# Optimization experiments

Measured on AMD Instinct MI355X. Metric: run time of the kernel, lower is better.

## Reference

```python
import jax, jax.numpy as jnp
import numpy as np

NUM_HEADS = 8
KEY_DIM = 512  # d_gain = 1/sqrt(key_dim) in the original (NOT per-head dim)
MASK_FILL = -1000000.0


def setup_inputs() -> dict:
    key = jax.random.key(0)
    ks = jax.random.split(key, 6)
    N, Tq, Tk, D, U = 8, 1024, 1024, 512, 512
    query = jax.random.normal(ks[0], (N, Tq, D), dtype=jnp.float32)
    key_t = jax.random.normal(ks[1], (N, Tk, D), dtype=jnp.float32)
    key_mask = jax.random.randint(ks[2], (N, Tk), 0, 2).astype(bool)
    Wq = jax.random.normal(ks[3], (D, U), dtype=jnp.float32) / np.sqrt(D)
    Wk = jax.random.normal(ks[4], (D, U), dtype=jnp.float32) / np.sqrt(D)
    Wv = jax.random.normal(ks[5], (D, U), dtype=jnp.float32) / np.sqrt(D)
    return {"query": query, "key": key_t, "key_mask": key_mask,
            "Wq": Wq, "Wk": Wk, "Wv": Wv}


def reference(query, key, key_mask, Wq, Wk, Wv):
    N, Tq, _ = query.shape
    Tk = key.shape[1]
    U = Wq.shape[1]
    h = NUM_HEADS
    d = U // h
    scale = 1.0 / (KEY_DIM ** 0.5)

    # projections then split heads: [N,T,U] -> [h,N,T,d]
    q = (query @ Wq).reshape(N, Tq, h, d).transpose(2, 0, 1, 3)
    k = (key @ Wk).reshape(N, Tk, h, d).transpose(2, 0, 1, 3)
    v = (key @ Wv).reshape(N, Tk, h, d).transpose(2, 0, 1, 3)

    scores = scale * jnp.einsum('hnqd,hnkd->hnqk', q, k)
    scores = jnp.where(key_mask[None, :, None, :], scores, MASK_FILL)
    attn = jax.nn.softmax(scores, axis=3)
    out = jnp.einsum('hnqk,hnkd->hnqd', attn, v)
    # merge heads: [h,N,Tq,d] -> [N,Tq,h*d]
    return out.transpose(1, 2, 0, 3).reshape(N, Tq, U)
```

## Files before the change

### kernel.cpp

```cpp
#include <hip/hip_runtime.h>
#include <hip/hip_bf16.h>

typedef unsigned short u16;
typedef __attribute__((ext_vector_type(8))) short short8;
typedef __attribute__((ext_vector_type(4))) short short4v;
typedef __attribute__((ext_vector_type(4))) float f32x4;

#define NB 8
#define TT 1024
#define DD 512
#define UU 512
#define HH 8
#define DH 64
#define SCALE 0.044194173824159216f
#define LOG2E 1.4426950408889634f
#define MASK_FILL_2 -1442695.0f

__device__ __forceinline__ float ld_flex(const void* p, long i, bool f32) {
  if (f32) return ((const float*)p)[i];
  unsigned int u = (unsigned int)(((const u16*)p)[i]) << 16;
  return __uint_as_float(u);
}

__device__ __forceinline__ u16 f32_to_bf16(float f) {
  unsigned int u = __float_as_uint(f);
  unsigned int r = (u + 0x7FFFu + ((u >> 16) & 1u)) >> 16;
  return (u16)r;
}

__device__ __forceinline__ float ex2(float x) {
#if __has_builtin(__builtin_amdgcn_exp2f)
  return __builtin_amdgcn_exp2f(x);
#else
  return __expf(x * 0.6931471805599453f);
#endif
}

__device__ __forceinline__ unsigned int pk_bf16(float a, float b) {
  union { __hip_bfloat162 h2; unsigned int u; } c;
  c.h2 = __float22bfloat162_rn(make_float2(a, b));
  return c.u;
}

__device__ __forceinline__ void gld16(const void* g, void* l) {
  __builtin_amdgcn_global_load_lds(
      (const __attribute__((address_space(1))) unsigned int*)g,
      (__attribute__((address_space(3))) unsigned int*)l, 16, 0, 0);
}

#define CONV_BLOCKS 8192
#define WT_BLOCKS 768
#define MASK_BLOCKS 32

__global__ __launch_bounds__(256) void prep_kernel(
    const void* __restrict__ query, const void* __restrict__ key,
    const void* __restrict__ W0, const void* __restrict__ W1,
    const void* __restrict__ W2, const void* __restrict__ mask,
    u16* __restrict__ Xq, u16* __restrict__ Xk, u16* __restrict__ Wt,
    float* __restrict__ maskadd, int* __restrict__ flags) {
  __shared__ float tile[32][33];
  __shared__ int s_f32, s_mi32;
  const int b = blockIdx.x, tid = threadIdx.x;

  if (tid == 0) { s_f32 = 0; s_mi32 = 1; }
  __syncthreads();
  {
    const u16* qh = (const u16*)query;
    int weird = 0;
#pragma unroll
    for (int p = 0; p < 4; ++p) {
      unsigned int u = (unsigned int)qh[tid * 4 + p] << 16;
      float v = __uint_as_float(u);
      if (!(v == v) || fabsf(v) > 1e6f) weird = 1;
    }
    if (weird) atomicOr(&s_f32, 1);
    const unsigned int* mi = (const unsigned int*)mask;
    if (mi[tid * 2] > 1u || mi[tid * 2 + 1] > 1u) atomicAnd(&s_mi32, 0);
  }
  __syncthreads();
  const bool f32 = s_f32 != 0;
  const bool mi32 = s_mi32 != 0;
  if (b == CONV_BLOCKS && tid == 0) { flags[0] = s_f32; flags[1] = s_mi32; }

  if (b < CONV_BLOCKS) {
    if (!f32) return;
    const void* in = (b < 4096) ? query : key;
    u16* out = (b < 4096) ? Xq : Xk;
    int i = (b & 4095) * 256 + tid;
    float4 v = ((const float4*)in)[i];
    ushort4 o;
    o.x = f32_to_bf16(v.x); o.y = f32_to_bf16(v.y);
    o.z = f32_to_bf16(v.z); o.w = f32_to_bf16(v.w);
    ((ushort4*)out)[i] = o;
  } else if (b < CONV_BLOCKS + WT_BLOCKS) {
    const int lb = b - CONV_BLOCKS;
    const int z = lb >> 8, rem = lb & 255;
    const int k0 = (rem & 15) * 32, n0 = (rem >> 4) * 32;
    const void* W = (z == 0) ? W0 : (z == 1) ? W1 : W2;
    const float sc = (z == 0) ? SCALE * LOG2E : 1.0f;
    u16* out = Wt + (size_t)z * DD * UU;
#pragma unroll
    for (int p = 0; p < 4; ++p) {
      int i = (tid >> 5) + p * 8, j = tid & 31;
      tile[i][j] = ld_flex(W, (long)(k0 + i) * UU + n0 + j, f32);
    }
    __syncthreads();
#pragma unroll
    for (int p = 0; p < 4; ++p) {
      int nl = (tid >> 5) + p * 8, kl = tid & 31;
      out[(size_t)(n0 + nl) * DD + k0 + kl] = f32_to_bf16(tile[kl][nl] * sc);
    }
  } else {
    const int i = (b - CONV_BLOCKS - WT_BLOCKS) * 256 + tid;
    bool mv = mi32 ? (((const int*)mask)[i] != 0)
                   : (((const unsigned char*)mask)[i] != 0);
    maskadd[i] = mv ? 0.0f : MASK_FILL_2;
  }
}

__global__ __launch_bounds__(256) void proj_mfma(
    const void* __restrict__ query, const void* __restrict__ key,
    const u16* __restrict__ Xq, const u16* __restrict__ Xk,
    const u16* __restrict__ Wt, u16* __restrict__ Qp, u16* __restrict__ Kp,
    u16* __restrict__ Vt, const int* __restrict__ flags) {
  __shared__ __align__(16) u16 smem[128 * 136];
  const bool f32 = flags[0] != 0;
  const int lid = blockIdx.x + (blockIdx.y << 6) + (blockIdx.z << 8);
  const int swz = (lid & 7) * 96 + (lid >> 3);
  const int bx = swz & 63, by = (swz >> 6) & 3, z = swz >> 8;
  const u16* X = (z == 0) ? (f32 ? Xq : (const u16*)query)
                          : (f32 ? Xk : (const u16*)key);
  const u16* Wz = Wt + (size_t)z * DD * UU;
  const int m0 = bx * 128, n0 = by * 128;
  const int tid = threadIdx.x;
  const int w = tid >> 6, l = tid & 63;
  const int quad = l >> 4, l15 = l & 15;
  const int wm = (w >> 1) * 64, wn = (w & 1) * 64;

  const int c0 = w * 128 + l;
  const int row0 = c0 >> 2, q0 = (c0 & 3) * 8;
  const int c1 = c0 + 64;
  const int row1 = c1 >> 2, q1 = (c1 & 3) * 8;
  const u16* aS0 = X + (size_t)(m0 + row0) * DD + q0;
  const u16* aS1 = X + (size_t)(m0 + row1) * DD + q1;
  const u16* bS0 = Wz + (size_t)(n0 + row0) * DD + q0;
  const u16* bS1 = Wz + (size_t)(n0 + row1) * DD + q1;
  const int dD0 = w * 1024;
  const int dD1 = w * 1024 + 512;

  f32x4 acc[4][4];
#pragma unroll
  for (int mi = 0; mi < 4; ++mi)
#pragma unroll
    for (int ni = 0; ni < 4; ++ni)
#pragma unroll
      for (int r = 0; r < 4; ++r) acc[mi][ni][r] = 0.0f;

  gld16(aS0, smem + dD0);
  gld16(aS1, smem + dD1);
  gld16(bS0, smem + 4096 + dD0);
  gld16(bS1, smem + 4096 + dD1);

#pragma unroll 1
  for (int t = 0; t < 16; ++t) {
    const int co = (t & 1) * 8192;
    if (t < 15) {
      const int k1 = (t + 1) * 32;
      const int no = ((t + 1) & 1) * 8192;
      gld16(aS0 + k1, smem + no + dD0);
      gld16(aS1 + k1, smem + no + dD1);
      gld16(bS0 + k1, smem + no + 4096 + dD0);
      gld16(bS1 + k1, smem + no + 4096 + dD1);
      asm volatile("s_waitcnt vmcnt(4)" ::: "memory");
    } else {
      asm volatile("s_waitcnt vmcnt(0)" ::: "memory");
    }
    __builtin_amdgcn_s_barrier();

    short8 af[4], bf[4];
#pragma unroll
    for (int mi = 0; mi < 4; ++mi)
      af[mi] = *(const short8*)&smem[co + (wm + mi * 16 + l15) * 32 + quad * 8];
#pragma unroll
    for (int ni = 0; ni < 4; ++ni)
      bf[ni] = *(const short8*)&smem[co + 4096 + (wn + ni * 16 + l15) * 32 + quad * 8];
#pragma unroll
    for (int mi = 0; mi < 4; ++mi)
#pragma unroll
      for (int ni = 0; ni < 4; ++ni)
        acc[mi][ni] = __builtin_amdgcn_mfma_f32_16x16x32_bf16(
            af[mi], bf[ni], acc[mi][ni], 0, 0, 0);
    __builtin_amdgcn_s_barrier();
  }

  if (z < 2) {
#pragma unroll
    for (int mi = 0; mi < 4; ++mi)
#pragma unroll
      for (int ni = 0; ni < 4; ++ni) {
        const int ml = wm + mi * 16 + quad * 4;
        const int nl = wn + ni * 16 + l15;
#pragma unroll
        for (int r = 0; r < 4; ++r)
          smem[(ml + r) * 136 + nl] = f32_to_bf16(acc[mi][ni][r]);
      }
  } else {
#pragma unroll
    for (int mi = 0; mi < 4; ++mi)
#pragma unroll
      for (int ni = 0; ni < 4; ++ni) {
        const int ml = wm + mi * 16 + quad * 4;
        const int nl = wn + ni * 16 + l15;
        ushort4 pk;
        pk.x = f32_to_bf16(acc[mi][ni][0]);
        pk.y = f32_to_bf16(acc[mi][ni][1]);
        pk.z = f32_to_bf16(acc[mi][ni][2]);
        pk.w = f32_to_bf16(acc[mi][ni][3]);
        *(ushort4*)&smem[nl * 136 + ml] = pk;
      }
  }
  __syncthreads();

  if (z < 2) {
    u16* outp = (z == 0) ? Qp : Kp;
#pragma unroll
    for (int p = 0; p < 8; ++p) {
      const int idx = tid + p * 256;
      const int row = idx >> 4, c8 = (idx & 15) * 8;
      short8 v = *(const short8*)&smem[row * 136 + c8];
      *(short8*)&outp[(size_t)(m0 + row) * UU + n0 + c8] = v;
    }
  } else {
    const int nb = m0 >> 10, tk0 = m0 & 1023;
#pragma unroll
    for (int p = 0; p < 8; ++p) {
      const int idx = tid + p * 256;
      const int row = idx >> 4, c8 = (idx & 15) * 8;
      const int u = n0 + row, h = u >> 6, dh = u & 63;
      short8 v = *(const short8*)&smem[row * 136 + c8];
      *(short8*)&Vt[(size_t)((nb * HH + h) * DH + dh) * TT + tk0 + c8] = v;
    }
  }
}

__global__ __launch_bounds__(256) void attn_mfma(
    const u16* __restrict__ Qp, const u16* __restrict__ Kp,
    const u16* __restrict__ Vt, const float* __restrict__ maskadd,
    void* __restrict__ out, const int* __restrict__ flags) {
  __shared__ __align__(16) char smem[23040];
  const int tid = threadIdx.x;
  const int w = tid >> 6, l = tid & 63;
  const int quad = l >> 4, l15 = l & 15;
  const int lid = blockIdx.x + (blockIdx.y << 4) + (blockIdx.z << 7);
  const int swz = (lid & 7) * 128 + (lid >> 3);
  const int qt = swz & 15, h = (swz >> 4) & 7, n = swz >> 7;
  const int qsub = w >> 1, ks = w & 1;
  const int q0 = qt * 64 + qsub * 32;
  const int kb0 = ks * 512;
  const bool f32o = flags[0] != 0;
  u16* Pw = (u16*)smem + w * 2304;
  float* lp = (float*)(smem + 18432);
  float* s_mask = (float*)(smem + 18944);

  ((float4*)s_mask)[tid] = ((const float4*)(maskadd + n * TT))[tid];

  const u16* qbase = Qp + (size_t)(n * TT + q0 + l15) * UU + h * DH + quad * 8;
  short8 bq[2][2];
  bq[0][0] = *(const short8*)(qbase);
  bq[0][1] = *(const short8*)(qbase + 32);
  bq[1][0] = *(const short8*)(qbase + 16 * UU);
  bq[1][1] = *(const short8*)(qbase + 16 * UU + 32);

  const u16* kbase = Kp + (size_t)(n * TT + l15) * UU + h * DH + quad * 8;
  const u16* vbase = Vt + (size_t)((n * HH + h) * DH + l15) * TT + quad * 8;

  f32x4 o[2][4];
  float lsum[2] = {0.0f, 0.0f};
#pragma unroll
  for (int nq = 0; nq < 2; ++nq)
#pragma unroll
    for (int ni = 0; ni < 4; ++ni)
#pragma unroll
      for (int r = 0; r < 4; ++r) o[nq][ni][r] = 0.0f;

  __syncthreads();

  short8 ak[2][2];
#pragma unroll
  for (int kt = 0; kt < 2; ++kt)
#pragma unroll
    for (int kd = 0; kd < 2; ++kd)
      ak[kt][kd] = *(const short8*)(kbase + (size_t)(kb0 + kt * 16) * UU + kd * 32);
  {
    f32x4 s[2][2];
#pragma unroll
    for (int kt = 0; kt < 2; ++kt)
#pragma unroll
      for (int nq = 0; nq < 2; ++nq) {
#pragma unroll
        for (int r = 0; r < 4; ++r) s[kt][nq][r] = 0.0f;
#pragma unroll
        for (int kd = 0; kd < 2; ++kd)
          s[kt][nq] = __builtin_amdgcn_mfma_f32_16x16x32_bf16(
              ak[kt][kd], bq[nq][kd], s[kt][nq], 0, 0, 0);
      }
#pragma unroll
    for (int kt = 0; kt < 2; ++kt)
#pragma unroll
      for (int kd = 0; kd < 2; ++kd)
        ak[kt][kd] = *(const short8*)(kbase + (size_t)(kb0 + 32 + kt * 16) * UU + kd * 32);
    float4 mk[2];
    mk[0] = *(const float4*)&s_mask[kb0 + quad * 4];
    mk[1] = *(const float4*)&s_mask[kb0 + 16 + quad * 4];
#pragma unroll
    for (int kt = 0; kt < 2; ++kt)
#pragma unroll
      for (int nq = 0; nq < 2; ++nq) {
        float e0 = ex2(s[kt][nq][0] + mk[kt].x);
        float e1 = ex2(s[kt][nq][1] + mk[kt].y);
        float e2 = ex2(s[kt][nq][2] + mk[kt].z);
        float e3 = ex2(s[kt][nq][3] + mk[kt].w);
        lsum[nq] += (e0 + e1) + (e2 + e3);
        uint2 pk = make_uint2(pk_bf16(e0, e1), pk_bf16(e2, e3));
        *(uint2*)&Pw[(nq * 16 + l15) * 36 + kt * 16 + quad * 4] = pk;
      }
  }

#pragma unroll 1
  for (int it = 0; it < 16; ++it) {
    const int kb = kb0 + it * 32;
    u16* Pr = Pw + (it & 1) * 1152;
    short8 ap[2];
#pragma unroll
    for (int nq = 0; nq < 2; ++nq) {
      short4v lo = *(const short4v*)&Pr[(nq * 16 + l15) * 36 + quad * 8];
      short4v hi = *(const short4v*)&Pr[(nq * 16 + l15) * 36 + quad * 8 + 4];
      union { short8 v8; short4v v4[2]; } u;
      u.v4[0] = lo; u.v4[1] = hi;
      ap[nq] = u.v8;
    }
    short8 vf[4];
#pragma unroll
    for (int ni = 0; ni < 4; ++ni)
      vf[ni] = *(const short8*)(vbase + (size_t)(ni * 16) * TT + kb);
    __builtin_amdgcn_sched_barrier(0);

    if (it < 15) {
      f32x4 s[2][2];
#pragma unroll
      for (int kt = 0; kt < 2; ++kt)
#pragma unroll
        for (int nq = 0; nq < 2; ++nq) {
#pragma unroll
          for (int r = 0; r < 4; ++r) s[kt][nq][r] = 0.0f;
#pragma unroll
          for (int kd = 0; kd < 2; ++kd)
            s[kt][nq] = __builtin_amdgcn_mfma_f32_16x16x32_bf16(
                ak[kt][kd], bq[nq][kd], s[kt][nq], 0, 0, 0);
        }
      if (it < 14) {
        const int kb2 = kb + 64;
#pragma unroll
        for (int kt = 0; kt < 2; ++kt)
#pragma unroll
          for (int kd = 0; kd < 2; ++kd)
            ak[kt][kd] = *(const short8*)(kbase + (size_t)(kb2 + kt * 16) * UU + kd * 32);
      }
      float4 mk[2];
      mk[0] = *(const float4*)&s_mask[kb + 32 + quad * 4];
      mk[1] = *(const float4*)&s_mask[kb + 48 + quad * 4];
      u16* Pn = Pw + ((it + 1) & 1) * 1152;
#pragma unroll
      for (int kt = 0; kt < 2; ++kt)
#pragma unroll
        for (int nq = 0; nq < 2; ++nq) {
          float e0 = ex2(s[kt][nq][0] + mk[kt].x);
          float e1 = ex2(s[kt][nq][1] + mk[kt].y);
          float e2 = ex2(s[kt][nq][2] + mk[kt].z);
          float e3 = ex2(s[kt][nq][3] + mk[kt].w);
          lsum[nq] += (e0 + e1) + (e2 + e3);
          uint2 pk = make_uint2(pk_bf16(e0, e1), pk_bf16(e2, e3));
          *(uint2*)&Pn[(nq * 16 + l15) * 36 + kt * 16 + quad * 4] = pk;
        }
    }
    __builtin_amdgcn_sched_barrier(0);

#pragma unroll
    for (int nq = 0; nq < 2; ++nq)
#pragma unroll
      for (int ni = 0; ni < 4; ++ni)
        o[nq][ni] = __builtin_amdgcn_mfma_f32_16x16x32_bf16(
            ap[nq], vf[ni], o[nq][ni], 0, 0, 0);
  }

#pragma unroll
  for (int nq = 0; nq < 2; ++nq) {
    lsum[nq] += __shfl_xor(lsum[nq], 16);
    lsum[nq] += __shfl_xor(lsum[nq], 32);
  }

  if (quad == 0) {
    lp[w * 32 + l15] = lsum[0];
    lp[w * 32 + 16 + l15] = lsum[1];
  }
  __syncthreads();

  float* cbuf = (float*)smem;
#pragma unroll
  for (int c = 0; c < 4; ++c) {
    if ((w >> 1) == (c >> 1)) {
      float* Ow = cbuf + (w & 1) * (16 * 68);
#pragma unroll
      for (int ni = 0; ni < 4; ++ni)
#pragma unroll
        for (int r = 0; r < 4; ++r)
          Ow[(quad * 4 + r) * 68 + ni * 16 + l15] = o[c & 1][ni][r];
    }
    __syncthreads();
    for (int i = tid; i < 16 * 64; i += 256) {
      int q = i >> 6, j = i & 63;
      float s = cbuf[q * 68 + j] + cbuf[1088 + q * 68 + j];
      int qg = c * 16 + q;
      int base = (c >> 1) * 64;
      float lsum2 = lp[base + (qg & 31)] + lp[base + 32 + (qg & 31)];
      float v = s / lsum2;
      size_t idx = (size_t)(n * TT + qt * 64 + qg) * UU + h * DH + j;
      if (f32o) ((float*)out)[idx] = v;
      else ((u16*)out)[idx] = f32_to_bf16(v);
    }
    __syncthreads();
  }
}

extern "C" void kernel_launch(void* const* d_in, const int* in_sizes, int n_in,
                              void* d_out, int out_size, void* d_ws, size_t ws_size,
                              hipStream_t stream) {
  const void* query = d_in[0];
  const void* key   = d_in[1];
  const void* mask  = d_in[2];
  const void* Wq    = d_in[3];
  const void* Wk    = d_in[4];
  const void* Wv    = d_in[5];

  char* base = (char*)d_ws;
  int* flags = (int*)base;
  float* maskadd = (float*)(base + 256);
  u16* Wt  = (u16*)(base + 64 * 1024);
  u16* Xq  = Wt + (size_t)3 * DD * UU;
  u16* Xk  = Xq + (size_t)NB * TT * DD;
  u16* Qp  = Xk + (size_t)NB * TT * DD;
  u16* Kp  = Qp + (size_t)NB * TT * UU;
  u16* Vtp = Kp + (size_t)NB * TT * UU;

  prep_kernel<<<CONV_BLOCKS + WT_BLOCKS + MASK_BLOCKS, 256, 0, stream>>>(
      query, key, Wq, Wk, Wv, mask, Xq, Xk, Wt, maskadd, flags);

  dim3 pgrid(NB * TT / 128, UU / 128, 3);
  proj_mfma<<<pgrid, 256, 0, stream>>>(query, key, Xq, Xk, Wt, Qp, Kp, Vtp, flags);

  dim3 agrid(TT / 64, HH, NB);
  attn_mfma<<<agrid, 256, 0, stream>>>(Qp, Kp, Vtp, maskadd, d_out, flags);
}
```

Before: 180.5 us.

## Stage K/V tiles in LDS with double-buffered async loads, drop split-K combine

The attention kernel is restructured so each of the 4 warps owns 16 query rows over the full key range, instead of 32 rows over half the keys. Each 32-key K tile and V tile is loaded once per block into XOR-swizzled, double-buffered LDS with direct global-to-LDS loads, rather than every warp fetching its own fragments from global memory. This removes redundant global traffic and the LDS-based cross-warp reduction epilogue, and outputs are written straight from registers. In exchange it adds two block barriers per 32-key step over 32 steps, and it requests 4 blocks per CU through launch bounds, which may constrain register allocation.

```diff
diff --git a/kernel.cpp b/kernel.cpp
--- a/kernel.cpp
+++ b/kernel.cpp
@@ -243,193 +243,138 @@
   }
 }
 
-__global__ __launch_bounds__(256) void attn_mfma(
+__global__ __launch_bounds__(256, 4) void attn_mfma(
     const u16* __restrict__ Qp, const u16* __restrict__ Kp,
     const u16* __restrict__ Vt, const float* __restrict__ maskadd,
     void* __restrict__ out, const int* __restrict__ flags) {
-  __shared__ __align__(16) char smem[23040];
+  __shared__ __align__(16) char smem[25344];
+  u16* sU = (u16*)smem;
   const int tid = threadIdx.x;
   const int w = tid >> 6, l = tid & 63;
   const int quad = l >> 4, l15 = l & 15;
   const int lid = blockIdx.x + (blockIdx.y << 4) + (blockIdx.z << 7);
   const int swz = (lid & 7) * 128 + (lid >> 3);
   const int qt = swz & 15, h = (swz >> 4) & 7, n = swz >> 7;
-  const int qsub = w >> 1, ks = w & 1;
-  const int q0 = qt * 64 + qsub * 32;
-  const int kb0 = ks * 512;
+  const int q0 = qt * 64;
   const bool f32o = flags[0] != 0;
-  u16* Pw = (u16*)smem + w * 2304;
-  float* lp = (float*)(smem + 18432);
-  float* s_mask = (float*)(smem + 18944);
+  u16* Pw = sU + 8192 + w * 576;
+  float* s_mask = (float*)(smem + 20992);
+  float* lp = (float*)(smem + 25088);
 
   ((float4*)s_mask)[tid] = ((const float4*)(maskadd + n * TT))[tid];
 
-  const u16* qbase = Qp + (size_t)(n * TT + q0 + l15) * UU + h * DH + quad * 8;
-  short8 bq[2][2];
-  bq[0][0] = *(const short8*)(qbase);
-  bq[0][1] = *(const short8*)(qbase + 32);
-  bq[1][0] = *(const short8*)(qbase + 16 * UU);
-  bq[1][1] = *(const short8*)(qbase + 16 * UU + 32);
-
-  const u16* kbase = Kp + (size_t)(n * TT + l15) * UU + h * DH + quad * 8;
-  const u16* vbase = Vt + (size_t)((n * HH + h) * DH + l15) * TT + quad * 8;
-
-  f32x4 o[2][4];
-  float lsum[2] = {0.0f, 0.0f};
-#pragma unroll
-  for (int nq = 0; nq < 2; ++nq)
+  const u16* qbase = Qp + (size_t)(n * TT + q0 + w * 16 + l15) * UU + h * DH + quad * 8;
+  short8 bq[2];
+  bq[0] = *(const short8*)(qbase);
+  bq[1] = *(const short8*)(qbase + 32);
+
+  const int lr3 = l >> 3, ls7 = l & 7;
+  const int lr2 = l >> 2, ls3 = l & 3;
+  const u16* kcur = Kp + (size_t)(n * TT + w * 8 + lr3) * UU + h * DH +
+                    ((ls7 ^ lr3) * 8);
+  const u16* vcur = Vt + (size_t)((n * HH + h) * DH + w * 16 + lr2) * TT +
+                    ((ls3 ^ (lr2 & 3)) * 8);
+
+  f32x4 o[4];
+  float lsum = 0.0f;
+#pragma unroll
+  for (int ni = 0; ni < 4; ++ni)
+#pragma unroll
+    for (int r = 0; r < 4; ++r) o[ni][r] = 0.0f;
+
+  __syncthreads();
+
+  gld16(kcur, smem + w * 1024);
+  gld16(vcur, smem + 8192 + w * 1024);
+
+#pragma unroll 1
+  for (int t = 0; t < 32; ++t) {
+    const int co = (t & 1) * 2048;
+    if (t < 31) {
+      const int no = ((t + 1) & 1) * 4096;
+      gld16(kcur + (size_t)(t + 1) * 32 * UU, smem + no + w * 1024);
+      gld16(vcur + (t + 1) * 32, smem + 8192 + no + w * 1024);
+      asm volatile("s_waitcnt vmcnt(2)" ::: "memory");
+    } else {
+      asm volatile("s_waitcnt vmcnt(0)" ::: "memory");
+    }
+    __builtin_amdgcn_s_barrier();
+
+    const int kb = t * 32;
+    short8 ak[2][2];
+#pragma unroll
+    for (int kt = 0; kt < 2; ++kt)
+#pragma unroll
+      for (int kd = 0; kd < 2; ++kd)
+        ak[kt][kd] = *(const short8*)&sU[co + (kt * 16 + l15) * 64 +
+                                         (((kd * 4 + quad) ^ (l15 & 7)) * 8)];
+    float4 mk0 = *(const float4*)&s_mask[kb + quad * 4];
+    float4 mk1 = *(const float4*)&s_mask[kb + 16 + quad * 4];
+
+    f32x4 s[2];
+#pragma unroll
+    for (int kt = 0; kt < 2; ++kt) {
+#pragma unroll
+      for (int r = 0; r < 4; ++r) s[kt][r] = 0.0f;
+#pragma unroll
+      for (int kd = 0; kd < 2; ++kd)
+        s[kt] = __builtin_amdgcn_mfma_f32_16x16x32_bf16(
+            ak[kt][kd], bq[kd], s[kt], 0, 0, 0);
+    }
+
+#pragma unroll
+    for (int kt = 0; kt < 2; ++kt) {
+      const float4 mk = kt ? mk1 : mk0;
+      float e0 = ex2(s[kt][0] + mk.x);
+      float e1 = ex2(s[kt][1] + mk.y);
+      float e2 = ex2(s[kt][2] + mk.z);
+      float e3 = ex2(s[kt][3] + mk.w);
+      lsum += (e0 + e1) + (e2 + e3);
+      uint2 pk = make_uint2(pk_bf16(e0, e1), pk_bf16(e2, e3));
+      *(uint2*)&Pw[l15 * 36 + kt * 16 + quad * 4] = pk;
+    }
+
+    short8 vf[4];
 #pragma unroll
     for (int ni = 0; ni < 4; ++ni)
-#pragma unroll
-      for (int r = 0; r < 4; ++r) o[nq][ni][r] = 0.0f;
-
-  __syncthreads();
-
-  short8 ak[2][2];
-#pragma unroll
-  for (int kt = 0; kt < 2; ++kt)
-#pragma unroll
-    for (int kd = 0; kd < 2; ++kd)
-      ak[kt][kd] = *(const short8*)(kbase + (size_t)(kb0 + kt * 16) * UU + kd * 32);
-  {
-    f32x4 s[2][2];
-#pragma unroll
-    for (int kt = 0; kt < 2; ++kt)
-#pragma unroll
-      for (int nq = 0; nq < 2; ++nq) {
-#pragma unroll
-        for (int r = 0; r < 4; ++r) s[kt][nq][r] = 0.0f;
-#pragma unroll
-        for (int kd = 0; kd < 2; ++kd)
-          s[kt][nq] = __builtin_amdgcn_mfma_f32_16x16x32_bf16(
-              ak[kt][kd], bq[nq][kd], s[kt][nq], 0, 0, 0);
-      }
-#pragma unroll
-    for (int kt = 0; kt < 2; ++kt)
-#pragma unroll
-      for (int kd = 0; kd < 2; ++kd)
-        ak[kt][kd] = *(const short8*)(kbase + (size_t)(kb0 + 32 + kt * 16) * UU + kd * 32);
-    float4 mk[2];
-    mk[0] = *(const float4*)&s_mask[kb0 + quad * 4];
-    mk[1] = *(const float4*)&s_mask[kb0 + 16 + quad * 4];
-#pragma unroll
-    for (int kt = 0; kt < 2; ++kt)
-#pragma unroll
-      for (int nq = 0; nq < 2; ++nq) {
-        float e0 = ex2(s[kt][nq][0] + mk[kt].x);
-        float e1 = ex2(s[kt][nq][1] + mk[kt].y);
-        float e2 = ex2(s[kt][nq][2] + mk[kt].z);
-        float e3 = ex2(s[kt][nq][3] + mk[kt].w);
-        lsum[nq] += (e0 + e1) + (e2 + e3);
-        uint2 pk = make_uint2(pk_bf16(e0, e1), pk_bf16(e2, e3));
-        *(uint2*)&Pw[(nq * 16 + l15) * 36 + kt * 16 + quad * 4] = pk;
-      }
-  }
-
-#pragma unroll 1
-  for (int it = 0; it < 16; ++it) {
-    const int kb = kb0 + it * 32;
-    u16* Pr = Pw + (it & 1) * 1152;
-    short8 ap[2];
-#pragma unroll
-    for (int nq = 0; nq < 2; ++nq) {
-      short4v lo = *(const short4v*)&Pr[(nq * 16 + l15) * 36 + quad * 8];
-      short4v hi = *(const short4v*)&Pr[(nq * 16 + l15) * 36 + quad * 8 + 4];
+      vf[ni] = *(const short8*)&sU[4096 + co + (ni * 16 + l15) * 32 +
+                                   ((quad ^ (l15 & 3)) * 8)];
+
+    short8 ap;
+    {
+      short4v lo = *(const short4v*)&Pw[l15 * 36 + quad * 8];
+      short4v hi = *(const short4v*)&Pw[l15 * 36 + quad * 8 + 4];
       union { short8 v8; short4v v4[2]; } u;
       u.v4[0] = lo; u.v4[1] = hi;
-      ap[nq] = u.v8;
-    }
-    short8 vf[4];
+      ap = u.v8;
+    }
+
 #pragma unroll
     for (int ni = 0; ni < 4; ++ni)
-      vf[ni] = *(const short8*)(vbase + (size_t)(ni * 16) * TT + kb);
-    __builtin_amdgcn_sched_barrier(0);
-
-    if (it < 15) {
-      f32x4 s[2][2];
-#pragma unroll
-      for (int kt = 0; kt < 2; ++kt)
-#pragma unroll
-        for (int nq = 0; nq < 2; ++nq) {
-#pragma unroll
-          for (int r = 0; r < 4; ++r) s[kt][nq][r] = 0.0f;
-#pragma unroll
-          for (int kd = 0; kd < 2; ++kd)
-            s[kt][nq] = __builtin_amdgcn_mfma_f32_16x16x32_bf16(
-                ak[kt][kd], bq[nq][kd], s[kt][nq], 0, 0, 0);
-        }
-      if (it < 14) {
-        const int kb2 = kb + 64;
-#pragma unroll
-        for (int kt = 0; kt < 2; ++kt)
-#pragma unroll
-          for (int kd = 0; kd < 2; ++kd)
-            ak[kt][kd] = *(const short8*)(kbase + (size_t)(kb2 + kt * 16) * UU + kd * 32);
-      }
-      float4 mk[2];
-      mk[0] = *(const float4*)&s_mask[kb + 32 + quad * 4];
-      mk[1] = *(const float4*)&s_mask[kb + 48 + quad * 4];
-      u16* Pn = Pw + ((it + 1) & 1) * 1152;
-#pragma unroll
-      for (int kt = 0; kt < 2; ++kt)
-#pragma unroll
-        for (int nq = 0; nq < 2; ++nq) {
-          float e0 = ex2(s[kt][nq][0] + mk[kt].x);
-          float e1 = ex2(s[kt][nq][1] + mk[kt].y);
-          float e2 = ex2(s[kt][nq][2] + mk[kt].z);
-          float e3 = ex2(s[kt][nq][3] + mk[kt].w);
-          lsum[nq] += (e0 + e1) + (e2 + e3);
-          uint2 pk = make_uint2(pk_bf16(e0, e1), pk_bf16(e2, e3));
-          *(uint2*)&Pn[(nq * 16 + l15) * 36 + kt * 16 + quad * 4] = pk;
-        }
-    }
-    __builtin_amdgcn_sched_barrier(0);
-
-#pragma unroll
-    for (int nq = 0; nq < 2; ++nq)
-#pragma unroll
-      for (int ni = 0; ni < 4; ++ni)
-        o[nq][ni] = __builtin_amdgcn_mfma_f32_16x16x32_bf16(
-            ap[nq], vf[ni], o[nq][ni], 0, 0, 0);
-  }
-
-#pragma unroll
-  for (int nq = 0; nq < 2; ++nq) {
-    lsum[nq] += __shfl_xor(lsum[nq], 16);
-    lsum[nq] += __shfl_xor(lsum[nq], 32);
-  }
-
-  if (quad == 0) {
-    lp[w * 32 + l15] = lsum[0];
-    lp[w * 32 + 16 + l15] = lsum[1];
-  }
+      o[ni] = __builtin_amdgcn_mfma_f32_16x16x32_bf16(ap, vf[ni], o[ni], 0, 0, 0);
+
+    __builtin_amdgcn_s_barrier();
+  }
+
+  lsum += __shfl_xor(lsum, 16);
+  lsum += __shfl_xor(lsum, 32);
+  if (l < 16) lp[w * 16 + l] = lsum;
   __syncthreads();
 
-  float* cbuf = (float*)smem;
-#pragma unroll
-  for (int c = 0; c < 4; ++c) {
-    if ((w >> 1) == (c >> 1)) {
-      float* Ow = cbuf + (w & 1) * (16 * 68);
-#pragma unroll
-      for (int ni = 0; ni < 4; ++ni)
-#pragma unroll
-        for (int r = 0; r < 4; ++r)
-          Ow[(quad * 4 + r) * 68 + ni * 16 + l15] = o[c & 1][ni][r];
-    }
-    __syncthreads();
-    for (int i = tid; i < 16 * 64; i += 256) {
-      int q = i >> 6, j = i & 63;
-      float s = cbuf[q * 68 + j] + cbuf[1088 + q * 68 + j];
-      int qg = c * 16 + q;
-      int base = (c >> 1) * 64;
-      float lsum2 = lp[base + (qg & 31)] + lp[base + 32 + (qg & 31)];
-      float v = s / lsum2;
-      size_t idx = (size_t)(n * TT + qt * 64 + qg) * UU + h * DH + j;
+  float den[4];
+#pragma unroll
+  for (int r = 0; r < 4; ++r) den[r] = lp[w * 16 + quad * 4 + r];
+
+#pragma unroll
+  for (int ni = 0; ni < 4; ++ni)
+#pragma unroll
+    for (int r = 0; r < 4; ++r) {
+      const int q = q0 + w * 16 + quad * 4 + r;
+      const float v = o[ni][r] / den[r];
+      const size_t idx = (size_t)(n * TT + q) * UU + h * DH + ni * 16 + l15;
       if (f32o) ((float*)out)[idx] = v;
       else ((u16*)out)[idx] = f32_to_bf16(v);
     }
-    __syncthreads();
-  }
 }
 
 extern "C" void kernel_launch(void* const* d_in, const int* in_sizes, int n_in,
```

New measurement: 149.9 us, median of 2. -17.0%, faster.
